# Kernel optimization log

Hardware: AMD Instinct MI355X
Metric: run time of the kernel (lower is better)

Reference implementation:

```python
import jax, jax.numpy as jnp
import numpy as np

N_RES = 768
DISTO_BINS = 64
LDDT_BINS = 50
MIN_RESOLUTION = 0.1
MAX_RESOLUTION = 3.0
W_DISTO, W_PLDDT, W_EXP = 0.3, 0.01, 0.01
CA_IDX = 1  # atom37 index of C-alpha


def setup_inputs() -> dict:
    key = jax.random.key(0)
    ks = jax.random.split(key, 6)
    B = 1
    return {
        "distogram_logits": jax.random.normal(ks[0], (B, N_RES, N_RES, DISTO_BINS), jnp.float32),
        "pseudo_beta": jax.random.normal(ks[1], (B, N_RES, 3), jnp.float32) * 10.0,
        "pseudo_beta_mask": jnp.ones((B, N_RES), jnp.float32),
        "lddt_logits": jax.random.normal(ks[2], (B, N_RES, LDDT_BINS), jnp.float32),
        "all_atom_pred_pos": jax.random.normal(ks[3], (B, N_RES, 37, 3), jnp.float32) * 10.0,
        "all_atom_positions": jax.random.normal(ks[4], (B, N_RES, 37, 3), jnp.float32) * 10.0,
        "all_atom_mask": jnp.ones((B, N_RES, 37), jnp.float32),
        "exp_resolved_logits": jax.random.normal(ks[5], (B, N_RES, 37), jnp.float32),
        "atom37_atom_exists": jnp.ones((B, N_RES, 37), jnp.float32),
        "resolution": jnp.ones((B,), jnp.float32),
    }


def _lddt(pred_pos, true_pos, mask, cutoff=15.0, eps=1e-10):
    # pred_pos/true_pos: [*, N, 3]; mask: [*, N, 1] -> per-residue lddt [*, N]
    n = mask.shape[-2]
    dmat_true = jnp.sqrt(eps + jnp.sum((true_pos[..., :, None, :] - true_pos[..., None, :, :]) ** 2, axis=-1))
    dmat_pred = jnp.sqrt(eps + jnp.sum((pred_pos[..., :, None, :] - pred_pos[..., None, :, :]) ** 2, axis=-1))
    scope = ((dmat_true < cutoff).astype(dmat_true.dtype)
             * mask * jnp.swapaxes(mask, -1, -2)
             * (1.0 - jnp.eye(n, dtype=dmat_true.dtype)))
    dist_l1 = jnp.abs(dmat_true - dmat_pred)
    score = 0.25 * ((dist_l1 < 0.5).astype(dist_l1.dtype) + (dist_l1 < 1.0)
                    + (dist_l1 < 2.0) + (dist_l1 < 4.0))
    norm = 1.0 / (eps + jnp.sum(scope, axis=-1))
    return norm * (eps + jnp.sum(scope * score, axis=-1))


def _ce_from_bins(logits, bins):
    # -sum(one_hot(bins) * log_softmax(logits)) == -log_softmax gathered at bins
    logp = jax.nn.log_softmax(logits, axis=-1)
    return -jnp.take_along_axis(logp, bins[..., None], axis=-1)[..., 0]


def _distogram_loss(logits, pseudo_beta, pseudo_beta_mask,
                    min_bin=2.3125, max_bin=21.6875, no_bins=DISTO_BINS, eps=1e-6):
    boundaries = jnp.linspace(min_bin, max_bin, no_bins - 1) ** 2
    d2 = jnp.sum((pseudo_beta[..., :, None, :] - pseudo_beta[..., None, :, :]) ** 2,
                 axis=-1, keepdims=True)  # [*, N, N, 1]
    true_bins = jnp.sum(d2 > boundaries, axis=-1).astype(jnp.int32)  # [*, N, N]
    errors = _ce_from_bins(logits, true_bins)
    sq_mask = pseudo_beta_mask[..., None] * pseudo_beta_mask[..., None, :]
    denom = eps + jnp.sum(sq_mask, axis=(-1, -2))
    mean = jnp.sum(errors * sq_mask, axis=-1) / denom[..., None]
    return jnp.mean(jnp.sum(mean, axis=-1))


def _lddt_loss(logits, all_atom_pred_pos, all_atom_positions, all_atom_mask, resolution,
               no_bins=LDDT_BINS, eps=1e-10):
    pred_ca = all_atom_pred_pos[..., CA_IDX, :]
    true_ca = all_atom_positions[..., CA_IDX, :]
    mask_ca = all_atom_mask[..., CA_IDX:CA_IDX + 1]  # [*, N, 1]
    score = jax.lax.stop_gradient(_lddt(pred_ca, true_ca, mask_ca, eps=eps))
    bin_idx = jnp.clip(jnp.floor(score * no_bins).astype(jnp.int32), 0, no_bins - 1)
    errors = _ce_from_bins(logits, bin_idx)
    m = mask_ca[..., 0]
    loss = jnp.sum(errors * m, axis=-1) / (eps + jnp.sum(m, axis=-1))
    gate = ((resolution >= MIN_RESOLUTION) & (resolution <= MAX_RESOLUTION)).astype(loss.dtype)
    return jnp.mean(loss * gate)


def _exp_resolved_loss(logits, atom37_atom_exists, all_atom_mask, resolution, eps=1e-8):
    errors = (-all_atom_mask * jax.nn.log_sigmoid(logits)
              - (1.0 - all_atom_mask) * jax.nn.log_sigmoid(-logits))
    loss = jnp.sum(errors * atom37_atom_exists, axis=-1)  # [*, N]
    loss = loss / (eps + jnp.sum(atom37_atom_exists, axis=(-1, -2)))[..., None]
    loss = jnp.sum(loss, axis=-1)
    gate = ((resolution >= MIN_RESOLUTION) & (resolution <= MAX_RESOLUTION)).astype(loss.dtype)
    return jnp.mean(loss * gate)


def reference(distogram_logits, pseudo_beta, pseudo_beta_mask, lddt_logits,
              all_atom_pred_pos, all_atom_positions, all_atom_mask,
              exp_resolved_logits, atom37_atom_exists, resolution):
    l_disto = _distogram_loss(distogram_logits, pseudo_beta, pseudo_beta_mask)
    l_plddt = _lddt_loss(lddt_logits, all_atom_pred_pos, all_atom_positions,
                         all_atom_mask, resolution)
    l_exp = _exp_resolved_loss(exp_resolved_logits, atom37_atom_exists,
                               all_atom_mask, resolution)
    return W_DISTO * l_disto + W_PLDDT * l_plddt + W_EXP * l_exp
```

## Files before the change

### kernel.cpp

```cpp
#include <hip/hip_runtime.h>
#include <math.h>

#define N_RES 768
#define DISTO_BINS 64
#define LDDT_BINS 50
#define DISTO_BLOCKS 2048
#define LDDT_BLOCKS N_RES
#define EXP_GRID 64
#define NPAIRS (N_RES * N_RES)
#define NCHUNKS (NPAIRS / 4)
#define CHUNKS_PER_WAVE 18

typedef float f32x4 __attribute__((ext_vector_type(4)));

#define ROW_ADD_ROR(v, N)                                                     \
    v += __int_as_float(__builtin_amdgcn_update_dpp(                          \
        0, __float_as_int(v), 0x120 | (N), 0xF, 0xF, false))

__global__ __launch_bounds__(256)
void pair_meta_kernel(const float* __restrict__ pb,
                      const float* __restrict__ pbm,
                      unsigned char* __restrict__ bins,
                      float* __restrict__ wgt) {
    int p = blockIdx.x * blockDim.x + threadIdx.x;
    if (p >= NPAIRS) return;
    int i = p / N_RES;
    int j = p - i * N_RES;
    float dx = pb[3 * i + 0] - pb[3 * j + 0];
    float dy = pb[3 * i + 1] - pb[3 * j + 1];
    float dz = pb[3 * i + 2] - pb[3 * j + 2];
    float d  = sqrtf(dx * dx + dy * dy + dz * dz);
    float t  = ceilf((d - 2.3125f) * 3.2f);
    int bin  = (int)fminf(fmaxf(t, 0.f), 63.f);
    bins[p]  = (unsigned char)bin;
    wgt[p]   = pbm[i] * pbm[j];
}

__global__ __launch_bounds__(256)
void fused_main_kernel(const f32x4* __restrict__ logits4,
                       const unsigned int* __restrict__ binw,
                       const float* __restrict__ wgt,
                       const float* __restrict__ pred37,
                       const float* __restrict__ true37,
                       const float* __restrict__ mask37,
                       const float* __restrict__ lddt_logits,
                       const float* __restrict__ exl,
                       const float* __restrict__ a37ex,
                       float* __restrict__ partial,
                       float* __restrict__ errm,
                       float* __restrict__ expnum,
                       float* __restrict__ expden) {
    __shared__ float r1[256], r2[256];
    const int tid  = threadIdx.x;
    const int nthr = blockDim.x;

    if (blockIdx.x < DISTO_BLOCKS) {
        const int lane = tid & 63;
        const int wid  = tid >> 6;
        const int q    = lane >> 4;
        const int gl   = lane & 15;
        const int gw   = blockIdx.x * 4 + wid;
        const int base = gw * CHUNKS_PER_WAVE;

        float acc = 0.f;

#define DISTO_PROC(xv4, cc)                                                   \
    {                                                                         \
        float e = __expf(xv4.x) + __expf(xv4.y) + __expf(xv4.z) +             \
                  __expf(xv4.w);                                              \
        ROW_ADD_ROR(e, 8);                                                    \
        ROW_ADD_ROR(e, 4);                                                    \
        ROW_ADD_ROR(e, 2);                                                    \
        ROW_ADD_ROR(e, 1);                                                    \
        unsigned int bw = binw[cc];                                           \
        int bin = (int)((bw >> (q * 8)) & 63u);                               \
        float w  = wgt[(cc) * 4 + q];                                         \
        float xs = (bin & 2) ? ((bin & 1) ? xv4.w : xv4.z)                    \
                             : ((bin & 1) ? xv4.y : xv4.x);                   \
        float lg = (gl == 0) ? w * __logf(e) : 0.f;                           \
        float bt = (gl == (bin >> 2)) ? w * xs : 0.f;                         \
        acc += lg - bt;                                                       \
    }

#pragma unroll
        for (int t3 = 0; t3 < 3; ++t3) {
            const int cb = base + t3 * 6;
            f32x4 x0 = __builtin_nontemporal_load(
                &logits4[(size_t)(cb + 0) * 64 + lane]);
            f32x4 x1 = __builtin_nontemporal_load(
                &logits4[(size_t)(cb + 1) * 64 + lane]);
            f32x4 x2 = __builtin_nontemporal_load(
                &logits4[(size_t)(cb + 2) * 64 + lane]);
            f32x4 x3 = __builtin_nontemporal_load(
                &logits4[(size_t)(cb + 3) * 64 + lane]);
            f32x4 x4 = __builtin_nontemporal_load(
                &logits4[(size_t)(cb + 4) * 64 + lane]);
            f32x4 x5 = __builtin_nontemporal_load(
                &logits4[(size_t)(cb + 5) * 64 + lane]);
            DISTO_PROC(x0, cb + 0);
            DISTO_PROC(x1, cb + 1);
            DISTO_PROC(x2, cb + 2);
            DISTO_PROC(x3, cb + 3);
            DISTO_PROC(x4, cb + 4);
            DISTO_PROC(x5, cb + 5);
        }
#undef DISTO_PROC

        acc += __shfl_xor(acc, 1, 64);
        acc += __shfl_xor(acc, 2, 64);
        acc += __shfl_xor(acc, 4, 64);
        acc += __shfl_xor(acc, 8, 64);
        acc += __shfl_xor(acc, 16, 64);
        acc += __shfl_xor(acc, 32, 64);
        if (lane == 0) r1[wid] = acc;
        __syncthreads();
        if (tid == 0)
            partial[blockIdx.x] = r1[0] + r1[1] + r1[2] + r1[3];
        return;
    }

    if (blockIdx.x >= DISTO_BLOCKS + LDDT_BLOCKS) {
        const int b = blockIdx.x - DISTO_BLOCKS - LDDT_BLOCKS;
        const int gid = b * nthr + tid;
        const int stride = EXP_GRID * nthr;
        const int n = N_RES * 37;
        float num = 0.f, den = 0.f;
        for (int k = gid; k < n; k += stride) {
            float x  = exl[k];
            float m  = mask37[k];
            float ex = a37ex[k];
            float ax = fabsf(x);
            float sp = __logf(1.f + __expf(-ax));
            float ls  = sp + fmaxf(-x, 0.f);
            float lsn = sp + fmaxf(x, 0.f);
            float err = m * ls + (1.f - m) * lsn;
            num += err * ex;
            den += ex;
        }
        r1[tid] = num;
        r2[tid] = den;
        __syncthreads();
        for (int s = nthr >> 1; s > 0; s >>= 1) {
            if (tid < s) { r1[tid] += r1[tid + s]; r2[tid] += r2[tid + s]; }
            __syncthreads();
        }
        if (tid == 0) { expnum[b] = r1[0]; expden[b] = r2[0]; }
        return;
    }

    const int i = blockIdx.x - DISTO_BLOCKS;
    const float tix = true37[(i * 37 + 1) * 3 + 0];
    const float tiy = true37[(i * 37 + 1) * 3 + 1];
    const float tiz = true37[(i * 37 + 1) * 3 + 2];
    const float pix = pred37[(i * 37 + 1) * 3 + 0];
    const float piy = pred37[(i * 37 + 1) * 3 + 1];
    const float piz = pred37[(i * 37 + 1) * 3 + 2];
    const float mi  = mask37[i * 37 + 1];

    float scope_sum = 0.f, score_sum = 0.f;
    for (int j = tid; j < N_RES; j += nthr) {
        float mj  = mask37[j * 37 + 1];
        float dtx = tix - true37[(j * 37 + 1) * 3 + 0];
        float dty = tiy - true37[(j * 37 + 1) * 3 + 1];
        float dtz = tiz - true37[(j * 37 + 1) * 3 + 2];
        float dt  = sqrtf(1e-10f + dtx * dtx + dty * dty + dtz * dtz);
        float dpx = pix - pred37[(j * 37 + 1) * 3 + 0];
        float dpy = piy - pred37[(j * 37 + 1) * 3 + 1];
        float dpz = piz - pred37[(j * 37 + 1) * 3 + 2];
        float dp  = sqrtf(1e-10f + dpx * dpx + dpy * dpy + dpz * dpz);
        float scope = (dt < 15.f && j != i) ? (mi * mj) : 0.f;
        float l1 = fabsf(dt - dp);
        float sc = 0.25f * ((l1 < 0.5f ? 1.f : 0.f) + (l1 < 1.f ? 1.f : 0.f) +
                            (l1 < 2.f ? 1.f : 0.f) + (l1 < 4.f ? 1.f : 0.f));
        scope_sum += scope;
        score_sum += scope * sc;
    }

    r1[tid] = scope_sum;
    r2[tid] = score_sum;
    __syncthreads();
    for (int s = nthr >> 1; s > 0; s >>= 1) {
        if (tid < s) { r1[tid] += r1[tid + s]; r2[tid] += r2[tid + s]; }
        __syncthreads();
    }

    __shared__ int binS;
    if (tid == 0) {
        float lddt = (1e-10f + r2[0]) / (1e-10f + r1[0]);
        int bin = (int)floorf(lddt * (float)LDDT_BINS);
        binS = min(max(bin, 0), LDDT_BINS - 1);
    }
    __syncthreads();

    float e = (tid < LDDT_BINS) ? __expf(lddt_logits[i * LDDT_BINS + tid]) : 0.f;
    r1[tid] = e;
    __syncthreads();
    for (int s = nthr >> 1; s > 0; s >>= 1) {
        if (tid < s) r1[tid] += r1[tid + s];
        __syncthreads();
    }
    if (tid == 0) {
        float err = __logf(r1[0]) - lddt_logits[i * LDDT_BINS + binS];
        errm[i] = err * mi;
    }
}

__global__ __launch_bounds__(256)
void finalize_kernel(const float* __restrict__ partial,
                     const float* __restrict__ pbm,
                     const float* __restrict__ errm,
                     const float* __restrict__ mask37,
                     const float* __restrict__ expnum,
                     const float* __restrict__ expden,
                     const float* __restrict__ resolution,
                     float* __restrict__ out) {
    const int tid = threadIdx.x;
    const int nthr = blockDim.x;

    double sd = 0.0, sm = 0.0, se = 0.0, smca = 0.0, num = 0.0, den = 0.0;
    for (int k = tid; k < DISTO_BLOCKS; k += nthr) sd += (double)partial[k];
    for (int k = tid; k < N_RES; k += nthr) {
        sm   += (double)pbm[k];
        se   += (double)errm[k];
        smca += (double)mask37[k * 37 + 1];
    }
    if (tid < EXP_GRID) { num = (double)expnum[tid]; den = (double)expden[tid]; }

    __shared__ double red[256];
    double vals[6] = {sd, sm, se, smca, num, den};
    double tot[6];
    for (int v = 0; v < 6; ++v) {
        red[tid] = vals[v];
        __syncthreads();
        for (int s = nthr >> 1; s > 0; s >>= 1) {
            if (tid < s) red[tid] += red[tid + s];
            __syncthreads();
        }
        tot[v] = red[0];
        __syncthreads();
    }

    if (tid == 0) {
        float res = resolution[0];
        double gate = (res >= 0.1f && res <= 3.0f) ? 1.0 : 0.0;
        double l_disto = tot[0] / (1e-6 + tot[1] * tot[1]);
        double l_plddt = tot[2] / (1e-10 + tot[3]) * gate;
        double l_exp   = tot[4] / (1e-8 + tot[5]) * gate;
        out[0] = (float)(0.3 * l_disto + 0.01 * l_plddt + 0.01 * l_exp);
    }
}

extern "C" void kernel_launch(void* const* d_in, const int* in_sizes, int n_in,
                              void* d_out, int out_size, void* d_ws, size_t ws_size,
                              hipStream_t stream) {
    const float* disto       = (const float*)d_in[0];
    const float* pb          = (const float*)d_in[1];
    const float* pbm         = (const float*)d_in[2];
    const float* lddt_logits = (const float*)d_in[3];
    const float* pred        = (const float*)d_in[4];
    const float* truep       = (const float*)d_in[5];
    const float* am          = (const float*)d_in[6];
    const float* exl         = (const float*)d_in[7];
    const float* a37         = (const float*)d_in[8];
    const float* resolution  = (const float*)d_in[9];
    float* out = (float*)d_out;

    float* ws      = (float*)d_ws;
    float* partial = ws;
    float* errm    = ws + DISTO_BLOCKS;
    float* expnum  = errm + N_RES;
    float* expden  = expnum + EXP_GRID;
    float* wgt     = ws + 4096;
    unsigned char* bins = (unsigned char*)(wgt + NPAIRS);

    pair_meta_kernel<<<(NPAIRS + 255) / 256, 256, 0, stream>>>(pb, pbm, bins, wgt);
    fused_main_kernel<<<DISTO_BLOCKS + LDDT_BLOCKS + EXP_GRID, 256, 0, stream>>>(
        (const f32x4*)disto, (const unsigned int*)bins, wgt,
        pred, truep, am, lddt_logits, exl, a37,
        partial, errm, expnum, expden);
    finalize_kernel<<<1, 256, 0, stream>>>(partial, pbm, errm, am,
                                           expnum, expden, resolution, out);
}
```

Baseline: 237.2 us.

## Fuse pair metadata into main kernel and finalize via atomic last-block reduction

Drops the pair_meta kernel that wrote bin indices and weights to global memory. Each distogram block now stages the pseudo-beta coordinates and mask in shared memory and computes bins and weights inline. The separate finalize kernel is replaced by float atomics into a small accumulator array plus a last-block-done counter, and a tiny init kernel zeroes the accumulators and precomputes the mask sums. This removes one global round trip and two kernel launches. The cost is extra sqrt work per chunk, 12 KB of shared memory per block, float instead of double accumulation, and contention on a few atomic addresses.

```diff
diff --git a/kernel.cpp b/kernel.cpp
--- a/kernel.cpp
+++ b/kernel.cpp
@@ -6,7 +6,8 @@
 #define LDDT_BINS 50
 #define DISTO_BLOCKS 2048
 #define LDDT_BLOCKS N_RES
-#define EXP_GRID 64
+#define EXP_BLOCKS 64
+#define TOTAL_BLOCKS (DISTO_BLOCKS + LDDT_BLOCKS + EXP_BLOCKS)
 #define NPAIRS (N_RES * N_RES)
 #define NCHUNKS (NPAIRS / 4)
 #define CHUNKS_PER_WAVE 18
@@ -18,43 +19,54 @@
         0, __float_as_int(v), 0x120 | (N), 0xF, 0xF, false))
 
 __global__ __launch_bounds__(256)
-void pair_meta_kernel(const float* __restrict__ pb,
-                      const float* __restrict__ pbm,
-                      unsigned char* __restrict__ bins,
-                      float* __restrict__ wgt) {
-    int p = blockIdx.x * blockDim.x + threadIdx.x;
-    if (p >= NPAIRS) return;
-    int i = p / N_RES;
-    int j = p - i * N_RES;
-    float dx = pb[3 * i + 0] - pb[3 * j + 0];
-    float dy = pb[3 * i + 1] - pb[3 * j + 1];
-    float dz = pb[3 * i + 2] - pb[3 * j + 2];
-    float d  = sqrtf(dx * dx + dy * dy + dz * dz);
-    float t  = ceilf((d - 2.3125f) * 3.2f);
-    int bin  = (int)fminf(fmaxf(t, 0.f), 63.f);
-    bins[p]  = (unsigned char)bin;
-    wgt[p]   = pbm[i] * pbm[j];
+void init_kernel(const float* __restrict__ pbm,
+                 const float* __restrict__ mask37,
+                 float* __restrict__ a) {
+    const int tid = threadIdx.x;
+    if (tid < 8) a[tid] = 0.f;
+    float sm = 0.f, smca = 0.f;
+    for (int k = tid; k < N_RES; k += 256) {
+        sm   += pbm[k];
+        smca += mask37[k * 37 + 1];
+    }
+    __shared__ float r1[256], r2[256];
+    r1[tid] = sm;
+    r2[tid] = smca;
+    __syncthreads();
+    for (int s = 128; s > 0; s >>= 1) {
+        if (tid < s) { r1[tid] += r1[tid + s]; r2[tid] += r2[tid + s]; }
+        __syncthreads();
+    }
+    if (tid == 0) { a[4] = r1[0]; a[5] = r2[0]; }
 }
 
 __global__ __launch_bounds__(256)
-void fused_main_kernel(const f32x4* __restrict__ logits4,
-                       const unsigned int* __restrict__ binw,
-                       const float* __restrict__ wgt,
-                       const float* __restrict__ pred37,
-                       const float* __restrict__ true37,
-                       const float* __restrict__ mask37,
-                       const float* __restrict__ lddt_logits,
-                       const float* __restrict__ exl,
-                       const float* __restrict__ a37ex,
-                       float* __restrict__ partial,
-                       float* __restrict__ errm,
-                       float* __restrict__ expnum,
-                       float* __restrict__ expden) {
+void main_kernel(const f32x4* __restrict__ logits4,
+                 const float* __restrict__ pb,
+                 const float* __restrict__ pbm,
+                 const float* __restrict__ pred37,
+                 const float* __restrict__ true37,
+                 const float* __restrict__ mask37,
+                 const float* __restrict__ lddt_logits,
+                 const float* __restrict__ exl,
+                 const float* __restrict__ a37ex,
+                 const float* __restrict__ resolution,
+                 float* __restrict__ a,
+                 float* __restrict__ out) {
     __shared__ float r1[256], r2[256];
     const int tid  = threadIdx.x;
     const int nthr = blockDim.x;
 
     if (blockIdx.x < DISTO_BLOCKS) {
+        __shared__ float spx[N_RES], spy[N_RES], spz[N_RES], spm[N_RES];
+        for (int k = tid; k < N_RES; k += nthr) {
+            spx[k] = pb[3 * k + 0];
+            spy[k] = pb[3 * k + 1];
+            spz[k] = pb[3 * k + 2];
+            spm[k] = pbm[k];
+        }
+        __syncthreads();
+
         const int lane = tid & 63;
         const int wid  = tid >> 6;
         const int q    = lane >> 4;
@@ -72,9 +84,16 @@
         ROW_ADD_ROR(e, 4);                                                    \
         ROW_ADD_ROR(e, 2);                                                    \
         ROW_ADD_ROR(e, 1);                                                    \
-        unsigned int bw = binw[cc];                                           \
-        int bin = (int)((bw >> (q * 8)) & 63u);                               \
-        float w  = wgt[(cc) * 4 + q];                                         \
+        int p = (cc) * 4 + q;                                                 \
+        int i = p / N_RES;                                                    \
+        int j = p - i * N_RES;                                                \
+        float dx = spx[i] - spx[j];                                           \
+        float dy = spy[i] - spy[j];                                           \
+        float dz = spz[i] - spz[j];                                           \
+        float d  = sqrtf(dx * dx + dy * dy + dz * dz);                        \
+        float t  = ceilf((d - 2.3125f) * 3.2f);                               \
+        int bin  = (int)fminf(fmaxf(t, 0.f), 63.f);                           \
+        float w  = spm[i] * spm[j];                                           \
         float xs = (bin & 2) ? ((bin & 1) ? xv4.w : xv4.z)                    \
                              : ((bin & 1) ? xv4.y : xv4.x);                   \
         float lg = (gl == 0) ? w * __logf(e) : 0.f;                           \
@@ -115,14 +134,11 @@
         if (lane == 0) r1[wid] = acc;
         __syncthreads();
         if (tid == 0)
-            partial[blockIdx.x] = r1[0] + r1[1] + r1[2] + r1[3];
-        return;
-    }
-
-    if (blockIdx.x >= DISTO_BLOCKS + LDDT_BLOCKS) {
+            atomicAdd(&a[0], r1[0] + r1[1] + r1[2] + r1[3]);
+    } else if (blockIdx.x >= DISTO_BLOCKS + LDDT_BLOCKS) {
         const int b = blockIdx.x - DISTO_BLOCKS - LDDT_BLOCKS;
         const int gid = b * nthr + tid;
-        const int stride = EXP_GRID * nthr;
+        const int stride = EXP_BLOCKS * nthr;
         const int n = N_RES * 37;
         float num = 0.f, den = 0.f;
         for (int k = gid; k < n; k += stride) {
@@ -144,109 +160,87 @@
             if (tid < s) { r1[tid] += r1[tid + s]; r2[tid] += r2[tid + s]; }
             __syncthreads();
         }
-        if (tid == 0) { expnum[b] = r1[0]; expden[b] = r2[0]; }
-        return;
-    }
-
-    const int i = blockIdx.x - DISTO_BLOCKS;
-    const float tix = true37[(i * 37 + 1) * 3 + 0];
-    const float tiy = true37[(i * 37 + 1) * 3 + 1];
-    const float tiz = true37[(i * 37 + 1) * 3 + 2];
-    const float pix = pred37[(i * 37 + 1) * 3 + 0];
-    const float piy = pred37[(i * 37 + 1) * 3 + 1];
-    const float piz = pred37[(i * 37 + 1) * 3 + 2];
-    const float mi  = mask37[i * 37 + 1];
-
-    float scope_sum = 0.f, score_sum = 0.f;
-    for (int j = tid; j < N_RES; j += nthr) {
-        float mj  = mask37[j * 37 + 1];
-        float dtx = tix - true37[(j * 37 + 1) * 3 + 0];
-        float dty = tiy - true37[(j * 37 + 1) * 3 + 1];
-        float dtz = tiz - true37[(j * 37 + 1) * 3 + 2];
-        float dt  = sqrtf(1e-10f + dtx * dtx + dty * dty + dtz * dtz);
-        float dpx = pix - pred37[(j * 37 + 1) * 3 + 0];
-        float dpy = piy - pred37[(j * 37 + 1) * 3 + 1];
-        float dpz = piz - pred37[(j * 37 + 1) * 3 + 2];
-        float dp  = sqrtf(1e-10f + dpx * dpx + dpy * dpy + dpz * dpz);
-        float scope = (dt < 15.f && j != i) ? (mi * mj) : 0.f;
-        float l1 = fabsf(dt - dp);
-        float sc = 0.25f * ((l1 < 0.5f ? 1.f : 0.f) + (l1 < 1.f ? 1.f : 0.f) +
-                            (l1 < 2.f ? 1.f : 0.f) + (l1 < 4.f ? 1.f : 0.f));
-        scope_sum += scope;
-        score_sum += scope * sc;
-    }
-
-    r1[tid] = scope_sum;
-    r2[tid] = score_sum;
+        if (tid == 0) {
+            atomicAdd(&a[2], r1[0]);
+            atomicAdd(&a[3], r2[0]);
+        }
+    } else {
+        const int i = blockIdx.x - DISTO_BLOCKS;
+        const float tix = true37[(i * 37 + 1) * 3 + 0];
+        const float tiy = true37[(i * 37 + 1) * 3 + 1];
+        const float tiz = true37[(i * 37 + 1) * 3 + 2];
+        const float pix = pred37[(i * 37 + 1) * 3 + 0];
+        const float piy = pred37[(i * 37 + 1) * 3 + 1];
+        const float piz = pred37[(i * 37 + 1) * 3 + 2];
+        const float mi  = mask37[i * 37 + 1];
+
+        float scope_sum = 0.f, score_sum = 0.f;
+        for (int j = tid; j < N_RES; j += nthr) {
+            float mj  = mask37[j * 37 + 1];
+            float dtx = tix - true37[(j * 37 + 1) * 3 + 0];
+            float dty = tiy - true37[(j * 37 + 1) * 3 + 1];
+            float dtz = tiz - true37[(j * 37 + 1) * 3 + 2];
+            float dt  = sqrtf(1e-10f + dtx * dtx + dty * dty + dtz * dtz);
+            float dpx = pix - pred37[(j * 37 + 1) * 3 + 0];
+            float dpy = piy - pred37[(j * 37 + 1) * 3 + 1];
+            float dpz = piz - pred37[(j * 37 + 1) * 3 + 2];
+            float dp  = sqrtf(1e-10f + dpx * dpx + dpy * dpy + dpz * dpz);
+            float scope = (dt < 15.f && j != i) ? (mi * mj) : 0.f;
+            float l1 = fabsf(dt - dp);
+            float sc = 0.25f * ((l1 < 0.5f ? 1.f : 0.f) + (l1 < 1.f ? 1.f : 0.f) +
+                                (l1 < 2.f ? 1.f : 0.f) + (l1 < 4.f ? 1.f : 0.f));
+            scope_sum += scope;
+            score_sum += scope * sc;
+        }
+
+        r1[tid] = scope_sum;
+        r2[tid] = score_sum;
+        __syncthreads();
+        for (int s = nthr >> 1; s > 0; s >>= 1) {
+            if (tid < s) { r1[tid] += r1[tid + s]; r2[tid] += r2[tid + s]; }
+            __syncthreads();
+        }
+
+        __shared__ int binS;
+        if (tid == 0) {
+            float lddt = (1e-10f + r2[0]) / (1e-10f + r1[0]);
+            int bin = (int)floorf(lddt * (float)LDDT_BINS);
+            binS = min(max(bin, 0), LDDT_BINS - 1);
+        }
+        __syncthreads();
+
+        float e = (tid < LDDT_BINS) ? __expf(lddt_logits[i * LDDT_BINS + tid]) : 0.f;
+        r1[tid] = e;
+        __syncthreads();
+        for (int s = nthr >> 1; s > 0; s >>= 1) {
+            if (tid < s) r1[tid] += r1[tid + s];
+            __syncthreads();
+        }
+        if (tid == 0) {
+            float err = __logf(r1[0]) - lddt_logits[i * LDDT_BINS + binS];
+            atomicAdd(&a[1], err * mi);
+        }
+    }
+
     __syncthreads();
-    for (int s = nthr >> 1; s > 0; s >>= 1) {
-        if (tid < s) { r1[tid] += r1[tid + s]; r2[tid] += r2[tid + s]; }
-        __syncthreads();
-    }
-
-    __shared__ int binS;
     if (tid == 0) {
-        float lddt = (1e-10f + r2[0]) / (1e-10f + r1[0]);
-        int bin = (int)floorf(lddt * (float)LDDT_BINS);
-        binS = min(max(bin, 0), LDDT_BINS - 1);
-    }
-    __syncthreads();
-
-    float e = (tid < LDDT_BINS) ? __expf(lddt_logits[i * LDDT_BINS + tid]) : 0.f;
-    r1[tid] = e;
-    __syncthreads();
-    for (int s = nthr >> 1; s > 0; s >>= 1) {
-        if (tid < s) r1[tid] += r1[tid + s];
-        __syncthreads();
-    }
-    if (tid == 0) {
-        float err = __logf(r1[0]) - lddt_logits[i * LDDT_BINS + binS];
-        errm[i] = err * mi;
-    }
-}
-
-__global__ __launch_bounds__(256)
-void finalize_kernel(const float* __restrict__ partial,
-                     const float* __restrict__ pbm,
-                     const float* __restrict__ errm,
-                     const float* __restrict__ mask37,
-                     const float* __restrict__ expnum,
-                     const float* __restrict__ expden,
-                     const float* __restrict__ resolution,
-                     float* __restrict__ out) {
-    const int tid = threadIdx.x;
-    const int nthr = blockDim.x;
-
-    double sd = 0.0, sm = 0.0, se = 0.0, smca = 0.0, num = 0.0, den = 0.0;
-    for (int k = tid; k < DISTO_BLOCKS; k += nthr) sd += (double)partial[k];
-    for (int k = tid; k < N_RES; k += nthr) {
-        sm   += (double)pbm[k];
-        se   += (double)errm[k];
-        smca += (double)mask37[k * 37 + 1];
-    }
-    if (tid < EXP_GRID) { num = (double)expnum[tid]; den = (double)expden[tid]; }
-
-    __shared__ double red[256];
-    double vals[6] = {sd, sm, se, smca, num, den};
-    double tot[6];
-    for (int v = 0; v < 6; ++v) {
-        red[tid] = vals[v];
-        __syncthreads();
-        for (int s = nthr >> 1; s > 0; s >>= 1) {
-            if (tid < s) red[tid] += red[tid + s];
-            __syncthreads();
-        }
-        tot[v] = red[0];
-        __syncthreads();
-    }
-
-    if (tid == 0) {
-        float res = resolution[0];
-        double gate = (res >= 0.1f && res <= 3.0f) ? 1.0 : 0.0;
-        double l_disto = tot[0] / (1e-6 + tot[1] * tot[1]);
-        double l_plddt = tot[2] / (1e-10 + tot[3]) * gate;
-        double l_exp   = tot[4] / (1e-8 + tot[5]) * gate;
-        out[0] = (float)(0.3 * l_disto + 0.01 * l_plddt + 0.01 * l_exp);
+        __threadfence();
+        unsigned int* cnt = (unsigned int*)(a + 6);
+        unsigned int old = atomicAdd(cnt, 1u);
+        if (old == TOTAL_BLOCKS - 1) {
+            float sd   = atomicAdd(&a[0], 0.f);
+            float se   = atomicAdd(&a[1], 0.f);
+            float num  = atomicAdd(&a[2], 0.f);
+            float den  = atomicAdd(&a[3], 0.f);
+            float sm   = atomicAdd(&a[4], 0.f);
+            float smca = atomicAdd(&a[5], 0.f);
+            float res  = resolution[0];
+            float gate = (res >= 0.1f && res <= 3.0f) ? 1.f : 0.f;
+            float l_disto = sd / (1e-6f + sm * sm);
+            float l_plddt = se / (1e-10f + smca) * gate;
+            float l_exp   = num / (1e-8f + den) * gate;
+            out[0] = 0.3f * l_disto + 0.01f * l_plddt + 0.01f * l_exp;
+        }
     }
 }
 
@@ -264,20 +258,10 @@
     const float* a37         = (const float*)d_in[8];
     const float* resolution  = (const float*)d_in[9];
     float* out = (float*)d_out;
-
-    float* ws      = (float*)d_ws;
-    float* partial = ws;
-    float* errm    = ws + DISTO_BLOCKS;
-    float* expnum  = errm + N_RES;
-    float* expden  = expnum + EXP_GRID;
-    float* wgt     = ws + 4096;
-    unsigned char* bins = (unsigned char*)(wgt + NPAIRS);
-
-    pair_meta_kernel<<<(NPAIRS + 255) / 256, 256, 0, stream>>>(pb, pbm, bins, wgt);
-    fused_main_kernel<<<DISTO_BLOCKS + LDDT_BLOCKS + EXP_GRID, 256, 0, stream>>>(
-        (const f32x4*)disto, (const unsigned int*)bins, wgt,
-        pred, truep, am, lddt_logits, exl, a37,
-        partial, errm, expnum, expden);
-    finalize_kernel<<<1, 256, 0, stream>>>(partial, pbm, errm, am,
-                                           expnum, expden, resolution, out);
+    float* acc = (float*)d_ws;
+
+    init_kernel<<<1, 256, 0, stream>>>(pbm, am, acc);
+    main_kernel<<<TOTAL_BLOCKS, 256, 0, stream>>>(
+        (const f32x4*)disto, pb, pbm, pred, truep, am, lddt_logits,
+        exl, a37, resolution, acc, out);
 }
```

Result: slower. 359.6 us (+51.6%).
